# Performance work log

Measured on AMD Instinct MI355X. Metric: run time of the kernel, lower is better.

## Reference

```python
import jax, jax.numpy as jnp
import numpy as np

N_NODES = 100000
N_EDGES = 300000
N_GRAPHS = 2048
F_ATOM = 40
D_IN = 128    # GINInputSize
D_HID = 256   # GINHiddenSize
D_OUT = 512   # FPSize
D_TASK = 1    # OutputSize


def _glorot(key, shape):
    fan_in, fan_out = shape[0], shape[1]
    lim = (6.0 / (fan_in + fan_out)) ** 0.5
    return jax.random.uniform(key, shape, jnp.float32, -lim, lim)


def setup_inputs() -> dict:
    key = jax.random.key(0)
    ks = jax.random.split(key, 16)
    inp = {
        'x': jax.random.normal(ks[0], (N_NODES, F_ATOM), jnp.float32),
        'edge_index': jax.random.randint(ks[1], (2, N_EDGES), 0, N_NODES, jnp.int64),
        'batch': jnp.sort(jax.random.randint(ks[2], (N_NODES,), 0, N_GRAPHS, jnp.int64)),
        # NodeFeatEmbed: MLP([F_ATOM, D_IN]) == single Linear (plain_last)
        'W_embed': _glorot(ks[3], (F_ATOM, D_IN)),
        'b_embed': jnp.zeros((D_IN,), jnp.float32),
        # GINConv eps per layer (train_eps=False -> 0.0 constants)
        'eps': jnp.zeros((3,), jnp.float32),
        # layer 0: MLP([D_IN, D_HID, D_HID])
        'W1_0': _glorot(ks[4], (D_IN, D_HID)),  'b1_0': jnp.zeros((D_HID,), jnp.float32),
        'W2_0': _glorot(ks[5], (D_HID, D_HID)), 'b2_0': jnp.zeros((D_HID,), jnp.float32),
        # layer 1: MLP([D_HID, D_HID, D_HID])
        'W1_1': _glorot(ks[6], (D_HID, D_HID)), 'b1_1': jnp.zeros((D_HID,), jnp.float32),
        'W2_1': _glorot(ks[7], (D_HID, D_HID)), 'b2_1': jnp.zeros((D_HID,), jnp.float32),
        # layer 2 (last, maps to out_channels=FPSize): MLP([D_HID, D_OUT, D_OUT])
        'W1_2': _glorot(ks[8], (D_HID, D_OUT)), 'b1_2': jnp.zeros((D_OUT,), jnp.float32),
        'W2_2': _glorot(ks[9], (D_OUT, D_OUT)), 'b2_2': jnp.zeros((D_OUT,), jnp.float32),
        # task head
        'W_task': _glorot(ks[10], (D_OUT, D_TASK)),
        'b_task': jnp.zeros((D_TASK,), jnp.float32),
    }
    return inp


def _gin_forward(x, edge_index, batch, W_embed, b_embed, eps, layers, W_task, b_task):
    src, dst = edge_index[0], edge_index[1]
    # NodeFeatEmbed
    h = x @ W_embed + b_embed                                    # [N, D_IN]
    n_layers = len(layers)
    for l, (W1, b1, W2, b2) in enumerate(layers):
        # GINConv: MLP((1+eps)*h + sum_{j->i} h_j)
        agg = jax.ops.segment_sum(h[src], dst, num_segments=N_NODES)
        z = (1.0 + eps[l]) * h + agg
        h = jax.nn.relu(z @ W1 + b1) @ W2 + b2
        if l < n_layers - 1:                                     # inter-layer act (not after last)
            h = jax.nn.relu(h)
    # global_add_pool readout
    pooled = jax.ops.segment_sum(h, batch, num_segments=N_GRAPHS)  # [G, D_OUT]
    return pooled @ W_task + b_task                               # [G, D_TASK]


def reference(x, edge_index, batch, W_embed, b_embed, eps,
              W1_0, b1_0, W2_0, b2_0,
              W1_1, b1_1, W2_1, b2_1,
              W1_2, b1_2, W2_2, b2_2,
              W_task, b_task):
    layers = [(W1_0, b1_0, W2_0, b2_0), (W1_1, b1_1, W2_1, b2_1), (W1_2, b1_2, W2_2, b2_2)]
    return _gin_forward(x, edge_index, batch, W_embed, b_embed, eps, layers, W_task, b_task)
```

## Files before the change

kernel.cpp:

```cpp
#include <hip/hip_runtime.h>

#define N_NODES 100000
#define E_EDGES 300000
#define N_GRAPHS 2048

typedef float  floatx4 __attribute__((ext_vector_type(4)));
typedef short  shortx8 __attribute__((ext_vector_type(8)));

__device__ __forceinline__ float bf2f(unsigned short u) {
  return __uint_as_float(((unsigned int)u) << 16);
}
__device__ __forceinline__ unsigned short f2bf(float f) {
  unsigned int u = __float_as_uint(f);
  u += 0x7FFFu + ((u >> 16) & 1u);
  return (unsigned short)(u >> 16);
}

__device__ __forceinline__ void cp16(const void* g, void* l) {
  __builtin_amdgcn_global_load_lds(
      (const __attribute__((address_space(1))) unsigned int*)g,
      (__attribute__((address_space(3))) unsigned int*)l, 16, 0, 0);
}

struct PrepArgs {
  const float* W[4];
  unsigned short* Wt[4];
  int K[4];
  int N[4];
  const float* We;
  const float* be;
  const float* W1_0;
  unsigned short* WfT;
  const float* W2_2;
  const float* b2_2;
  const float* wtask;
  float* w2v;
  float* c2;
  float* nodedot;
  float* out;
  const float* b_task;
};

__global__ __launch_bounds__(256)
void prep_kernel(PrepArgs a) {
  const int blk = blockIdx.x;
  if (blk < 320) {
    int z, b;
    if (blk < 64)       { z = 0; b = blk; }
    else if (blk < 128) { z = 1; b = blk - 64; }
    else if (blk < 192) { z = 2; b = blk - 128; }
    else                { z = 3; b = blk - 192; }
    const int K = a.K[z], N = a.N[z];
    const int nt = N / 32;
    const int kb = (b / nt) * 32, nb = (b % nt) * 32;
    __shared__ unsigned short tile[32][33];
    const float* W = a.W[z];
    unsigned short* Wt = a.Wt[z];
    const int tx = threadIdx.x & 31, ty = threadIdx.x >> 5;
    for (int r = ty; r < 32; r += 8)
      tile[r][tx] = f2bf(W[(size_t)(kb + r) * N + nb + tx]);
    __syncthreads();
    for (int r = ty; r < 32; r += 8)
      Wt[(size_t)(nb + r) * K + kb + tx] = tile[tx][r];
  } else if (blk < 361) {
    const int k = blk - 320;
    const int n = threadIdx.x;
    if (k < 40) {
      float s = 0.f;
      for (int j = 0; j < 128; j++) s = fmaf(a.We[k * 128 + j], a.W1_0[(size_t)j * 256 + n], s);
      a.WfT[n * 64 + k] = f2bf(s);
    } else {
      float s = 0.f;
      for (int j = 0; j < 128; j++) s = fmaf(a.be[j], a.W1_0[(size_t)j * 256 + n], s);
      a.WfT[n * 64 + 40] = f2bf(s);
      for (int kk = 41; kk < 64; kk++) a.WfT[n * 64 + kk] = 0;
    }
  } else if (blk < 490) {
    const int p = blk - 361;
    const int lane = threadIdx.x & 63;
    const int wave = threadIdx.x >> 6;
    if (p < 128) {
      const int k = p * 4 + wave;
      const float* row = a.W2_2 + (size_t)k * 512 + lane * 8;
      float4 a0 = *(const float4*)(row);
      float4 a1 = *(const float4*)(row + 4);
      float4 w0 = *(const float4*)(a.wtask + lane * 8);
      float4 w1 = *(const float4*)(a.wtask + lane * 8 + 4);
      float s = a0.x * w0.x + a0.y * w0.y + a0.z * w0.z + a0.w * w0.w +
                a1.x * w1.x + a1.y * w1.y + a1.z * w1.z + a1.w * w1.w;
#pragma unroll
      for (int off = 32; off > 0; off >>= 1) s += __shfl_down(s, off);
      if (lane == 0) a.w2v[k] = s;
    } else if (wave == 0) {
      float4 a0 = *(const float4*)(a.b2_2 + lane * 8);
      float4 a1 = *(const float4*)(a.b2_2 + lane * 8 + 4);
      float4 w0 = *(const float4*)(a.wtask + lane * 8);
      float4 w1 = *(const float4*)(a.wtask + lane * 8 + 4);
      float s = a0.x * w0.x + a0.y * w0.y + a0.z * w0.z + a0.w * w0.w +
                a1.x * w1.x + a1.y * w1.y + a1.z * w1.z + a1.w * w1.w;
#pragma unroll
      for (int off = 32; off > 0; off >>= 1) s += __shfl_down(s, off);
      if (lane == 0) *a.c2 = s;
    }
  } else if (blk < 881) {
    int i = (blk - 490) * 256 + threadIdx.x;
    if (i < N_NODES) a.nodedot[i] = 0.f;
  } else {
    int g = (blk - 881) * 256 + threadIdx.x;
    if (g < N_GRAPHS) a.out[g] = a.b_task[0];
  }
}

__global__ __launch_bounds__(256)
void zero_kernel(int* __restrict__ p, int n) {
  int i = blockIdx.x * 256 + threadIdx.x;
  if (i < n) p[i] = 0;
}

__global__ __launch_bounds__(256)
void hist_kernel(const int* __restrict__ ei, int* __restrict__ deg) {
  int e = blockIdx.x * 256 + threadIdx.x;
  if (e < E_EDGES) atomicAdd(&deg[ei[E_EDGES + e]], 1);
}

__global__ __launch_bounds__(256)
void scan_blk_kernel(const int* __restrict__ in, int* __restrict__ out,
                     int* __restrict__ blk_sums, int n_in, int n_out) {
  __shared__ int sm[256];
  const int t = threadIdx.x;
  const int base = blockIdx.x * 1024 + t * 4;
  int d0 = (base + 0 < n_in) ? in[base + 0] : 0;
  int d1 = (base + 1 < n_in) ? in[base + 1] : 0;
  int d2 = (base + 2 < n_in) ? in[base + 2] : 0;
  int d3 = (base + 3 < n_in) ? in[base + 3] : 0;
  int s = d0 + d1 + d2 + d3;
  sm[t] = s;
  __syncthreads();
  for (int off = 1; off < 256; off <<= 1) {
    int v = (t >= off) ? sm[t - off] : 0;
    __syncthreads();
    sm[t] += v;
    __syncthreads();
  }
  int excl = sm[t] - s;
  if (base + 0 < n_out) out[base + 0] = excl;
  if (base + 1 < n_out) out[base + 1] = excl + d0;
  if (base + 2 < n_out) out[base + 2] = excl + d0 + d1;
  if (base + 3 < n_out) out[base + 3] = excl + d0 + d1 + d2;
  if (t == 255 && blk_sums) blk_sums[blockIdx.x] = sm[255];
}

__global__ __launch_bounds__(256)
void scan_fix_kernel(int* __restrict__ row_ptr, const int* __restrict__ blk_off,
                     int* __restrict__ cursor) {
  int i = blockIdx.x * 256 + threadIdx.x;
  if (i <= N_NODES) {
    int v = row_ptr[i] + blk_off[i >> 10];
    row_ptr[i] = v;
    if (i < N_NODES) cursor[i] = v;
  }
}

__global__ __launch_bounds__(256)
void fill_kernel(const int* __restrict__ ei, int* __restrict__ cursor,
                 int* __restrict__ csr_src) {
  int e = blockIdx.x * 256 + threadIdx.x;
  if (e < E_EDGES) {
    int d = ei[E_EDGES + e];
    int slot = atomicAdd(&cursor[d], 1);
    csr_src[slot] = ei[e];
  }
}

__global__ __launch_bounds__(256)
void gatherx_kernel(const float* __restrict__ X, unsigned short* __restrict__ G,
                    const int* __restrict__ row_ptr, const int* __restrict__ csr,
                    const float* __restrict__ eps) {
  const int node = blockIdx.x * 4 + (threadIdx.x >> 6);
  const int lane = threadIdx.x & 63;
  const float sc = 1.0f + eps[0];
  const int e0 = row_ptr[node];
  const int e1 = row_ptr[node + 1];
  float acc = 0.f;
  if (lane < 40) {
    acc = sc * X[(size_t)node * 40 + lane];
    int e = e0;
    for (; e + 4 <= e1; e += 4) {
      int s0 = csr[e], s1 = csr[e + 1], s2 = csr[e + 2], s3 = csr[e + 3];
      float a0 = X[(size_t)s0 * 40 + lane];
      float a1 = X[(size_t)s1 * 40 + lane];
      float a2 = X[(size_t)s2 * 40 + lane];
      float a3 = X[(size_t)s3 * 40 + lane];
      acc += (a0 + a1) + (a2 + a3);
    }
    for (; e < e1; e++)
      acc += X[(size_t)csr[e] * 40 + lane];
  } else if (lane == 40) {
    acc = sc + (float)(e1 - e0);
  }
  G[(size_t)node * 64 + lane] = f2bf(acc);
}

__global__ __launch_bounds__(256)
void gather_kernel(const unsigned short* __restrict__ H, unsigned short* __restrict__ Z,
                   const int* __restrict__ row_ptr, const int* __restrict__ csr,
                   const float* __restrict__ eps, int l) {
  const int node = blockIdx.x * 4 + (threadIdx.x >> 6);
  const int lane = threadIdx.x & 63;
  const float sc = 1.0f + eps[l];
  uint2 hv = *(const uint2*)(H + (size_t)node * 256 + lane * 4);
  float acc[4];
  acc[0] = sc * bf2f((unsigned short)(hv.x & 0xFFFF));
  acc[1] = sc * bf2f((unsigned short)(hv.x >> 16));
  acc[2] = sc * bf2f((unsigned short)(hv.y & 0xFFFF));
  acc[3] = sc * bf2f((unsigned short)(hv.y >> 16));
  const int e0 = row_ptr[node];
  const int e1 = row_ptr[node + 1];
  int e = e0;
  for (; e + 2 <= e1; e += 2) {
    int s0 = csr[e], s1 = csr[e + 1];
    uint2 a = *(const uint2*)(H + (size_t)s0 * 256 + lane * 4);
    uint2 b = *(const uint2*)(H + (size_t)s1 * 256 + lane * 4);
    acc[0] += bf2f((unsigned short)(a.x & 0xFFFF)) + bf2f((unsigned short)(b.x & 0xFFFF));
    acc[1] += bf2f((unsigned short)(a.x >> 16))    + bf2f((unsigned short)(b.x >> 16));
    acc[2] += bf2f((unsigned short)(a.y & 0xFFFF)) + bf2f((unsigned short)(b.y & 0xFFFF));
    acc[3] += bf2f((unsigned short)(a.y >> 16))    + bf2f((unsigned short)(b.y >> 16));
  }
  if (e < e1) {
    int s0 = csr[e];
    uint2 a = *(const uint2*)(H + (size_t)s0 * 256 + lane * 4);
    acc[0] += bf2f((unsigned short)(a.x & 0xFFFF));
    acc[1] += bf2f((unsigned short)(a.x >> 16));
    acc[2] += bf2f((unsigned short)(a.y & 0xFFFF));
    acc[3] += bf2f((unsigned short)(a.y >> 16));
  }
  unsigned short z[4] = {f2bf(acc[0]), f2bf(acc[1]), f2bf(acc[2]), f2bf(acc[3])};
  *(uint2*)(Z + (size_t)node * 256 + lane * 4) = *(uint2*)z;
}

template <int K, int NXL, int MODE>
__global__ __launch_bounds__(256, 4)
void gemm_kernel(const unsigned short* __restrict__ A,
                 const unsigned short* __restrict__ Bt,
                 const float* __restrict__ bias, unsigned short* __restrict__ C,
                 const float* __restrict__ w2v, float* __restrict__ nodedot,
                 int M, int N) {
  const int g = blockIdx.x;
  const int mblk = ((g >> (3 + NXL)) << 3) | (g & 7);
  const int nblk = (g >> 3) & ((1 << NXL) - 1);
  const int m0 = mblk * 128;
  const int n0 = nblk * 128;
  if (m0 >= M) return;

  __shared__ unsigned short smem[2 * 128 * 64];
  unsigned short* As = smem;
  unsigned short* Bs = smem + 128 * 64;
  const int tid = threadIdx.x;
  const int lane = tid & 63;
  const int wave = tid >> 6;
  const int wm = (wave & 1) * 64;
  const int wn = (wave >> 1) * 64;
  const int fr = lane & 15;
  const int fq = lane >> 4;

  floatx4 acc[4][4];
#pragma unroll
  for (int i = 0; i < 4; i++)
#pragma unroll
    for (int j = 0; j < 4; j++) acc[i][j] = (floatx4){0.f, 0.f, 0.f, 0.f};

  const unsigned short* gA[4];
  const unsigned short* gB[4];
  unsigned short* lA[4];
  unsigned short* lB[4];
#pragma unroll
  for (int p = 0; p < 4; p++) {
    int c = p * 256 + wave * 64 + lane;
    int row = c >> 3;
    int q = (c & 7) ^ (row & 7);
    int grA = m0 + row;
    if (grA >= M) grA = M - 1;
    gA[p] = A + (size_t)grA * K + q * 8;
    gB[p] = Bt + (size_t)(n0 + row) * K + q * 8;
    lA[p] = &As[(p * 256 + wave * 64) * 8];
    lB[p] = &Bs[(p * 256 + wave * 64) * 8];
  }

  for (int k0 = 0; k0 < K; k0 += 64) {
#pragma unroll
    for (int p = 0; p < 4; p++) cp16(gA[p] + k0, lA[p]);
#pragma unroll
    for (int p = 0; p < 4; p++) cp16(gB[p] + k0, lB[p]);
    __syncthreads();
#pragma unroll
    for (int s0 = 0; s0 < 2; s0++) {
      shortx8 af[4], bf[4];
#pragma unroll
      for (int i = 0; i < 4; i++)
        af[i] = *(const shortx8*)&As[(wm + i * 16 + fr) * 64 +
                                     (((s0 * 4 + fq) ^ (fr & 7)) * 8)];
#pragma unroll
      for (int j = 0; j < 4; j++)
        bf[j] = *(const shortx8*)&Bs[(wn + j * 16 + fr) * 64 +
                                     (((s0 * 4 + fq) ^ (fr & 7)) * 8)];
#pragma unroll
      for (int i = 0; i < 4; i++)
#pragma unroll
        for (int j = 0; j < 4; j++)
          acc[i][j] = __builtin_amdgcn_mfma_f32_16x16x32_bf16(af[i], bf[j], acc[i][j], 0, 0, 0);
    }
    __syncthreads();
  }

  if (MODE == 3) {
    float wv[4], bj[4];
#pragma unroll
    for (int j = 0; j < 4; j++) {
      int col = n0 + wn + j * 16 + fr;
      wv[j] = w2v[col];
      bj[j] = bias[col];
    }
#pragma unroll
    for (int i = 0; i < 4; i++) {
#pragma unroll
      for (int r = 0; r < 4; r++) {
        float p = 0.f;
#pragma unroll
        for (int j = 0; j < 4; j++) p += fmaxf(acc[i][j][r] + bj[j], 0.f) * wv[j];
#pragma unroll
        for (int off = 1; off < 16; off <<= 1) p += __shfl_xor(p, off);
        if (fr == 0) {
          int row = m0 + wm + i * 16 + fq * 4 + r;
          if (row < M) unsafeAtomicAdd(&nodedot[row], p);
        }
      }
    }
  } else {
    unsigned short* Cs = smem;
#pragma unroll
    for (int j = 0; j < 4; j++) {
      int col = wn + j * 16 + fr;
      float bj = bias[n0 + col];
#pragma unroll
      for (int i = 0; i < 4; i++) {
#pragma unroll
        for (int r = 0; r < 4; r++) {
          int row = wm + i * 16 + fq * 4 + r;
          Cs[row * 128 + col] = f2bf(fmaxf(acc[i][j][r] + bj, 0.f));
        }
      }
    }
    __syncthreads();
    const int rcol = (tid & 15) * 8;
#pragma unroll
    for (int p = 0; p < 8; p++) {
      int row = p * 16 + (tid >> 4);
      int grow = m0 + row;
      if (grow < M) {
        uint4 v = *(const uint4*)&Cs[row * 128 + rcol];
        *(uint4*)&C[(size_t)grow * N + n0 + rcol] = v;
      }
    }
  }
}

__global__ __launch_bounds__(256)
void pool_kernel(const float* __restrict__ nodedot, const int* __restrict__ batch,
                 float* __restrict__ out, const float* __restrict__ c2p) {
  int t = blockIdx.x * 256 + threadIdx.x;
  int i0 = t * 64;
  if (i0 >= N_NODES) return;
  int i1 = i0 + 64;
  if (i1 > N_NODES) i1 = N_NODES;
  const float c2 = *c2p;
  int g = batch[i0];
  float s = 0.f;
  for (int i = i0; i < i1; i++) {
    int gi = batch[i];
    if (gi != g) { unsafeAtomicAdd(&out[g], s); g = gi; s = 0.f; }
    s += nodedot[i] + c2;
  }
  unsafeAtomicAdd(&out[g], s);
}

extern "C" void kernel_launch(void* const* d_in, const int* in_sizes, int n_in,
                              void* d_out, int out_size, void* d_ws, size_t ws_size,
                              hipStream_t stream) {
  const float* x       = (const float*)d_in[0];
  const int*   ei      = (const int*)d_in[1];
  const int*   batch   = (const int*)d_in[2];
  const float* W_embed = (const float*)d_in[3];
  const float* b_embed = (const float*)d_in[4];
  const float* eps     = (const float*)d_in[5];
  const float* W1[3] = {(const float*)d_in[6],  (const float*)d_in[10], (const float*)d_in[14]};
  const float* B1[3] = {(const float*)d_in[7],  (const float*)d_in[11], (const float*)d_in[15]};
  const float* W2[3] = {(const float*)d_in[8],  (const float*)d_in[12], (const float*)d_in[16]};
  const float* B2[3] = {(const float*)d_in[9],  (const float*)d_in[13], (const float*)d_in[17]};
  const float* W_task = (const float*)d_in[18];
  const float* b_task = (const float*)d_in[19];
  float* out = (float*)d_out;

  const size_t OFF_RB  = 51200000;
  const size_t OFF_RZ  = 102400000;
  const size_t OFF_AUX = 153600000;
  if (ws_size < OFF_AUX + 4000000) return;
  unsigned short* RH = (unsigned short*)d_ws;
  unsigned short* RB = (unsigned short*)((char*)d_ws + OFF_RB);
  unsigned short* RZ = (unsigned short*)((char*)d_ws + OFF_RZ);
  char* aux = (char*)d_ws + OFF_AUX;
  int* row_ptr  = (int*)(aux);
  int* cursor   = (int*)(aux + 400016);
  int* csr_src  = (int*)(aux + 800016);
  int* blk_sums = (int*)(aux + 2000016);
  int* blk_off  = (int*)(aux + 2000416);
  float* nodedot = (float*)(aux + 2000816);
  unsigned short* WT = (unsigned short*)(aux + 2400832);
  float* w2v = (float*)(aux + 3200832);
  float* c2  = (float*)(aux + 3202880);
  unsigned short* WfT    = WT;
  unsigned short* Wt2_0  = WT + 32768;
  unsigned short* Wt1_1  = WT + 98304;
  unsigned short* Wt2_1  = WT + 163840;
  unsigned short* Wt1_2  = WT + 229376;

  PrepArgs pa;
  pa.W[0] = W2[0]; pa.Wt[0] = Wt2_0; pa.K[0] = 256; pa.N[0] = 256;
  pa.W[1] = W1[1]; pa.Wt[1] = Wt1_1; pa.K[1] = 256; pa.N[1] = 256;
  pa.W[2] = W2[1]; pa.Wt[2] = Wt2_1; pa.K[2] = 256; pa.N[2] = 256;
  pa.W[3] = W1[2]; pa.Wt[3] = Wt1_2; pa.K[3] = 256; pa.N[3] = 512;
  pa.We = W_embed; pa.be = b_embed; pa.W1_0 = W1[0]; pa.WfT = WfT;
  pa.W2_2 = W2[2]; pa.b2_2 = B2[2]; pa.wtask = W_task; pa.w2v = w2v; pa.c2 = c2;
  pa.nodedot = nodedot; pa.out = out; pa.b_task = b_task;
  prep_kernel<<<889, 256, 0, stream>>>(pa);

  zero_kernel<<<(N_NODES + 255) / 256, 256, 0, stream>>>(cursor, N_NODES);
  hist_kernel<<<(E_EDGES + 255) / 256, 256, 0, stream>>>(ei, cursor);
  scan_blk_kernel<<<98, 256, 0, stream>>>(cursor, row_ptr, blk_sums, N_NODES, N_NODES + 1);
  scan_blk_kernel<<<1, 256, 0, stream>>>(blk_sums, blk_off, nullptr, 98, 98);
  scan_fix_kernel<<<(N_NODES + 256) / 256, 256, 0, stream>>>(row_ptr, blk_off, cursor);
  fill_kernel<<<(E_EDGES + 255) / 256, 256, 0, stream>>>(ei, cursor, csr_src);

  const int MB = (N_NODES + 127) / 128;
  const int MB8 = ((MB + 7) / 8) * 8;

  gatherx_kernel<<<N_NODES / 4, 256, 0, stream>>>(x, RZ, row_ptr, csr_src, eps);
  gemm_kernel<64, 1, 0><<<2 * MB8, 256, 0, stream>>>(RZ, WfT, B1[0], RB, nullptr, nullptr, N_NODES, 256);
  gemm_kernel<256, 1, 0><<<2 * MB8, 256, 0, stream>>>(RB, Wt2_0, B2[0], RH, nullptr, nullptr, N_NODES, 256);

  gather_kernel<<<N_NODES / 4, 256, 0, stream>>>(RH, RZ, row_ptr, csr_src, eps, 1);
  gemm_kernel<256, 1, 0><<<2 * MB8, 256, 0, stream>>>(RZ, Wt1_1, B1[1], RB, nullptr, nullptr, N_NODES, 256);
  gemm_kernel<256, 1, 0><<<2 * MB8, 256, 0, stream>>>(RB, Wt2_1, B2[1], RH, nullptr, nullptr, N_NODES, 256);

  gather_kernel<<<N_NODES / 4, 256, 0, stream>>>(RH, RZ, row_ptr, csr_src, eps, 2);
  gemm_kernel<256, 2, 3><<<4 * MB8, 256, 0, stream>>>(RZ, Wt1_2, B1[2], nullptr, w2v, nodedot, N_NODES, 512);

  pool_kernel<<<((N_NODES + 63) / 64 + 255) / 256, 256, 0, stream>>>(nodedot, batch, out, c2);
}
```

Measured before the change: 439.7 us.

## Fuse two-layer MLP GEMMs per 64-row tile keeping hidden activations in LDS

Replaces the pair of separate GEMM launches per GIN layer with a single kernel that computes relu(zW1+b1) for a 64-row tile, stores it in shared memory, then multiplies by W2 without writing the intermediate to global memory. The last layer is likewise rewritten so each block covers all 512 output columns and reduces the node dot product in registers, which means one atomic per row instead of one per column tile. This removes the intermediate HBM round trip and some launches. In exchange, tiles are smaller (64 rows, full N), weights are re-streamed through LDS in 32-wide K chunks with two barriers each, and occupancy drops to 3 blocks per CU.

```diff
diff --git a/kernel.cpp b/kernel.cpp
--- a/kernel.cpp
+++ b/kernel.cpp
@@ -238,30 +238,59 @@
   *(uint2*)(Z + (size_t)node * 256 + lane * 4) = *(uint2*)z;
 }
 
-template <int K, int NXL, int MODE>
-__global__ __launch_bounds__(256, 4)
-void gemm_kernel(const unsigned short* __restrict__ A,
-                 const unsigned short* __restrict__ Bt,
-                 const float* __restrict__ bias, unsigned short* __restrict__ C,
-                 const float* __restrict__ w2v, float* __restrict__ nodedot,
-                 int M, int N) {
-  const int g = blockIdx.x;
-  const int mblk = ((g >> (3 + NXL)) << 3) | (g & 7);
-  const int nblk = (g >> 3) & ((1 << NXL) - 1);
-  const int m0 = mblk * 128;
-  const int n0 = nblk * 128;
-  if (m0 >= M) return;
-
-  __shared__ unsigned short smem[2 * 128 * 64];
-  unsigned short* As = smem;
-  unsigned short* Bs = smem + 128 * 64;
+template <int K1>
+__global__ __launch_bounds__(256, 3)
+void fused_mlp_kernel(const unsigned short* __restrict__ A,
+                      const unsigned short* __restrict__ W1t,
+                      const float* __restrict__ b1,
+                      const unsigned short* __restrict__ W2t,
+                      const float* __restrict__ b2,
+                      unsigned short* __restrict__ H,
+                      int M) {
+  constexpr int ACH = K1 / 8;
+  constexpr int ZP = (64 * ACH) / 256;
+
+  __shared__ uint4 smem4[3072];
+  unsigned short* Bs = (unsigned short*)smem4;
+  unsigned short* Ts = (unsigned short*)(smem4 + 1024);
+
+  const int m0 = blockIdx.x * 64;
   const int tid = threadIdx.x;
   const int lane = tid & 63;
   const int wave = tid >> 6;
-  const int wm = (wave & 1) * 64;
-  const int wn = (wave >> 1) * 64;
   const int fr = lane & 15;
   const int fq = lane >> 4;
+  const int wn = wave * 64;
+
+#pragma unroll
+  for (int p = 0; p < ZP; p++) {
+    int slot = p * 256 + tid;
+    int row = slot / ACH;
+    int cs = slot % ACH;
+    int cg = cs ^ (row & 7);
+    int grow = m0 + row;
+    if (grow >= M) grow = M - 1;
+    cp16(A + (size_t)grow * K1 + cg * 8, Ts + (size_t)(p * 256 + wn) * 8);
+  }
+
+  const int bn_ = tid >> 2;
+  const int bc_ = tid & 3;
+  const unsigned short* srcW1[4];
+  const unsigned short* srcW2[4];
+#pragma unroll
+  for (int p = 0; p < 4; p++) {
+    int n = p * 64 + bn_;
+    int sw = (bc_ ^ ((n >> 1) & 3)) << 3;
+    srcW1[p] = W1t + (size_t)n * K1 + sw;
+    srcW2[p] = W2t + (size_t)n * 256 + sw;
+  }
+
+  int offB[4];
+#pragma unroll
+  for (int j = 0; j < 4; j++) {
+    int n = wn + j * 16 + fr;
+    offB[j] = n * 32 + ((fq ^ ((n >> 1) & 3)) << 3);
+  }
 
   floatx4 acc[4][4];
 #pragma unroll
@@ -269,99 +298,197 @@
 #pragma unroll
     for (int j = 0; j < 4; j++) acc[i][j] = (floatx4){0.f, 0.f, 0.f, 0.f};
 
-  const unsigned short* gA[4];
-  const unsigned short* gB[4];
-  unsigned short* lA[4];
-  unsigned short* lB[4];
+  for (int k0 = 0; k0 < K1; k0 += 32) {
+#pragma unroll
+    for (int p = 0; p < 4; p++)
+      cp16(srcW1[p] + k0, Bs + (size_t)(p * 256 + wn) * 8);
+    __syncthreads();
+    shortx8 af[4], bv[4];
+    const int kc = k0 >> 3;
+#pragma unroll
+    for (int i = 0; i < 4; i++) {
+      int row = i * 16 + fr;
+      af[i] = *(const shortx8*)&Ts[row * K1 + (((kc + fq) ^ (fr & 7)) << 3)];
+    }
+#pragma unroll
+    for (int j = 0; j < 4; j++) bv[j] = *(const shortx8*)&Bs[offB[j]];
+#pragma unroll
+    for (int i = 0; i < 4; i++)
+#pragma unroll
+      for (int j = 0; j < 4; j++)
+        acc[i][j] = __builtin_amdgcn_mfma_f32_16x16x32_bf16(af[i], bv[j], acc[i][j], 0, 0, 0);
+    __syncthreads();
+  }
+
+#pragma unroll
+  for (int j = 0; j < 4; j++) {
+    int col = wn + j * 16 + fr;
+    float bb = b1[col];
+    int cgc = col >> 3, c7 = col & 7;
+#pragma unroll
+    for (int i = 0; i < 4; i++)
+#pragma unroll
+      for (int r = 0; r < 4; r++) {
+        int row = i * 16 + fq * 4 + r;
+        float v = fmaxf(acc[i][j][r] + bb, 0.f);
+        Ts[row * 256 + (((cgc ^ (row & 7)) << 3) | c7)] = f2bf(v);
+        acc[i][j][r] = 0.f;
+      }
+  }
+
+  for (int k0 = 0; k0 < 256; k0 += 32) {
+#pragma unroll
+    for (int p = 0; p < 4; p++)
+      cp16(srcW2[p] + k0, Bs + (size_t)(p * 256 + wn) * 8);
+    __syncthreads();
+    shortx8 af[4], bv[4];
+    const int kc = k0 >> 3;
+#pragma unroll
+    for (int i = 0; i < 4; i++) {
+      int row = i * 16 + fr;
+      af[i] = *(const shortx8*)&Ts[row * 256 + (((kc + fq) ^ (fr & 7)) << 3)];
+    }
+#pragma unroll
+    for (int j = 0; j < 4; j++) bv[j] = *(const shortx8*)&Bs[offB[j]];
+#pragma unroll
+    for (int i = 0; i < 4; i++)
+#pragma unroll
+      for (int j = 0; j < 4; j++)
+        acc[i][j] = __builtin_amdgcn_mfma_f32_16x16x32_bf16(af[i], bv[j], acc[i][j], 0, 0, 0);
+    __syncthreads();
+  }
+
+#pragma unroll
+  for (int j = 0; j < 4; j++) {
+    int col = wn + j * 16 + fr;
+    float bb = b2[col];
+    int cgc = col >> 3, c7 = col & 7;
+#pragma unroll
+    for (int i = 0; i < 4; i++)
+#pragma unroll
+      for (int r = 0; r < 4; r++) {
+        int row = i * 16 + fq * 4 + r;
+        float v = fmaxf(acc[i][j][r] + bb, 0.f);
+        Ts[row * 256 + (((cgc ^ (row & 7)) << 3) | c7)] = f2bf(v);
+      }
+  }
+  __syncthreads();
+  const int r2 = tid >> 5;
+  const int cg2 = tid & 31;
+#pragma unroll
+  for (int p = 0; p < 8; p++) {
+    int row = p * 8 + r2;
+    int grow = m0 + row;
+    if (grow < M) {
+      uint4 v = *(const uint4*)&Ts[row * 256 + ((cg2 ^ (row & 7)) << 3)];
+      *(uint4*)&H[(size_t)grow * 256 + cg2 * 8] = v;
+    }
+  }
+}
+
+__global__ __launch_bounds__(256, 3)
+void fused_dot_kernel(const unsigned short* __restrict__ A,
+                      const unsigned short* __restrict__ W1t,
+                      const float* __restrict__ b1,
+                      const float* __restrict__ w2v,
+                      float* __restrict__ nodedot, int M) {
+  __shared__ uint4 smem4[3072];
+  unsigned short* Bs = (unsigned short*)smem4;
+  unsigned short* Ts = (unsigned short*)(smem4 + 1024);
+
+  const int m0 = blockIdx.x * 64;
+  const int tid = threadIdx.x;
+  const int lane = tid & 63;
+  const int wave = tid >> 6;
+  const int fr = lane & 15;
+  const int fq = lane >> 4;
+  const int wn = wave * 64;
+
+#pragma unroll
+  for (int p = 0; p < 8; p++) {
+    int slot = p * 256 + tid;
+    int row = slot >> 5;
+    int cs = slot & 31;
+    int cg = cs ^ (row & 7);
+    int grow = m0 + row;
+    if (grow >= M) grow = M - 1;
+    cp16(A + (size_t)grow * 256 + cg * 8, Ts + (size_t)(p * 256 + wn) * 8);
+  }
+
+  const int bn_ = tid >> 2;
+  const int bc_ = tid & 3;
+  const unsigned short* srcW[4];
 #pragma unroll
   for (int p = 0; p < 4; p++) {
-    int c = p * 256 + wave * 64 + lane;
-    int row = c >> 3;
-    int q = (c & 7) ^ (row & 7);
-    int grA = m0 + row;
-    if (grA >= M) grA = M - 1;
-    gA[p] = A + (size_t)grA * K + q * 8;
-    gB[p] = Bt + (size_t)(n0 + row) * K + q * 8;
-    lA[p] = &As[(p * 256 + wave * 64) * 8];
-    lB[p] = &Bs[(p * 256 + wave * 64) * 8];
-  }
-
-  for (int k0 = 0; k0 < K; k0 += 64) {
-#pragma unroll
-    for (int p = 0; p < 4; p++) cp16(gA[p] + k0, lA[p]);
-#pragma unroll
-    for (int p = 0; p < 4; p++) cp16(gB[p] + k0, lB[p]);
-    __syncthreads();
-#pragma unroll
-    for (int s0 = 0; s0 < 2; s0++) {
-      shortx8 af[4], bf[4];
+    int n = p * 64 + bn_;
+    srcW[p] = W1t + (size_t)n * 256 + ((bc_ ^ ((n >> 1) & 3)) << 3);
+  }
+  int offB[4];
+#pragma unroll
+  for (int j = 0; j < 4; j++) {
+    int n = wn + j * 16 + fr;
+    offB[j] = n * 32 + ((fq ^ ((n >> 1) & 3)) << 3);
+  }
+
+  float pd[4][4];
+#pragma unroll
+  for (int i = 0; i < 4; i++)
+#pragma unroll
+    for (int r = 0; r < 4; r++) pd[i][r] = 0.f;
+
+  for (int nh = 0; nh < 2; nh++) {
+    floatx4 acc[4][4];
+#pragma unroll
+    for (int i = 0; i < 4; i++)
+#pragma unroll
+      for (int j = 0; j < 4; j++) acc[i][j] = (floatx4){0.f, 0.f, 0.f, 0.f};
+    const size_t nhoff = (size_t)nh * 256 * 256;
+    for (int k0 = 0; k0 < 256; k0 += 32) {
+#pragma unroll
+      for (int p = 0; p < 4; p++)
+        cp16(srcW[p] + nhoff + k0, Bs + (size_t)(p * 256 + wn) * 8);
+      __syncthreads();
+      shortx8 af[4], bv[4];
+      const int kc = k0 >> 3;
+#pragma unroll
+      for (int i = 0; i < 4; i++) {
+        int row = i * 16 + fr;
+        af[i] = *(const shortx8*)&Ts[row * 256 + (((kc + fq) ^ (fr & 7)) << 3)];
+      }
+#pragma unroll
+      for (int j = 0; j < 4; j++) bv[j] = *(const shortx8*)&Bs[offB[j]];
 #pragma unroll
       for (int i = 0; i < 4; i++)
-        af[i] = *(const shortx8*)&As[(wm + i * 16 + fr) * 64 +
-                                     (((s0 * 4 + fq) ^ (fr & 7)) * 8)];
-#pragma unroll
-      for (int j = 0; j < 4; j++)
-        bf[j] = *(const shortx8*)&Bs[(wn + j * 16 + fr) * 64 +
-                                     (((s0 * 4 + fq) ^ (fr & 7)) * 8)];
+#pragma unroll
+        for (int j = 0; j < 4; j++)
+          acc[i][j] = __builtin_amdgcn_mfma_f32_16x16x32_bf16(af[i], bv[j], acc[i][j], 0, 0, 0);
+      __syncthreads();
+    }
+#pragma unroll
+    for (int j = 0; j < 4; j++) {
+      int col = nh * 256 + wn + j * 16 + fr;
+      float bb = b1[col];
+      float wv = w2v[col];
 #pragma unroll
       for (int i = 0; i < 4; i++)
 #pragma unroll
-        for (int j = 0; j < 4; j++)
-          acc[i][j] = __builtin_amdgcn_mfma_f32_16x16x32_bf16(af[i], bf[j], acc[i][j], 0, 0, 0);
-    }
-    __syncthreads();
-  }
-
-  if (MODE == 3) {
-    float wv[4], bj[4];
-#pragma unroll
-    for (int j = 0; j < 4; j++) {
-      int col = n0 + wn + j * 16 + fr;
-      wv[j] = w2v[col];
-      bj[j] = bias[col];
-    }
-#pragma unroll
-    for (int i = 0; i < 4; i++) {
-#pragma unroll
-      for (int r = 0; r < 4; r++) {
-        float p = 0.f;
-#pragma unroll
-        for (int j = 0; j < 4; j++) p += fmaxf(acc[i][j][r] + bj[j], 0.f) * wv[j];
-#pragma unroll
-        for (int off = 1; off < 16; off <<= 1) p += __shfl_xor(p, off);
-        if (fr == 0) {
-          int row = m0 + wm + i * 16 + fq * 4 + r;
-          if (row < M) unsafeAtomicAdd(&nodedot[row], p);
-        }
+        for (int r = 0; r < 4; r++)
+          pd[i][r] += fmaxf(acc[i][j][r] + bb, 0.f) * wv;
+    }
+  }
+
+#pragma unroll
+  for (int i = 0; i < 4; i++)
+#pragma unroll
+    for (int r = 0; r < 4; r++) {
+      float s = pd[i][r];
+#pragma unroll
+      for (int off = 1; off < 16; off <<= 1) s += __shfl_xor(s, off);
+      if (fr == 0) {
+        int row = m0 + i * 16 + fq * 4 + r;
+        if (row < M) unsafeAtomicAdd(&nodedot[row], s);
       }
     }
-  } else {
-    unsigned short* Cs = smem;
-#pragma unroll
-    for (int j = 0; j < 4; j++) {
-      int col = wn + j * 16 + fr;
-      float bj = bias[n0 + col];
-#pragma unroll
-      for (int i = 0; i < 4; i++) {
-#pragma unroll
-        for (int r = 0; r < 4; r++) {
-          int row = wm + i * 16 + fq * 4 + r;
-          Cs[row * 128 + col] = f2bf(fmaxf(acc[i][j][r] + bj, 0.f));
-        }
-      }
-    }
-    __syncthreads();
-    const int rcol = (tid & 15) * 8;
-#pragma unroll
-    for (int p = 0; p < 8; p++) {
-      int row = p * 16 + (tid >> 4);
-      int grow = m0 + row;
-      if (grow < M) {
-        uint4 v = *(const uint4*)&Cs[row * 128 + rcol];
-        *(uint4*)&C[(size_t)grow * N + n0 + rcol] = v;
-      }
-    }
-  }
 }
 
 __global__ __launch_bounds__(256)
@@ -400,12 +527,10 @@
   const float* b_task = (const float*)d_in[19];
   float* out = (float*)d_out;
 
-  const size_t OFF_RB  = 51200000;
   const size_t OFF_RZ  = 102400000;
   const size_t OFF_AUX = 153600000;
   if (ws_size < OFF_AUX + 4000000) return;
   unsigned short* RH = (unsigned short*)d_ws;
-  unsigned short* RB = (unsigned short*)((char*)d_ws + OFF_RB);
   unsigned short* RZ = (unsigned short*)((char*)d_ws + OFF_RZ);
   char* aux = (char*)d_ws + OFF_AUX;
   int* row_ptr  = (int*)(aux);
@@ -440,19 +565,16 @@
   scan_fix_kernel<<<(N_NODES + 256) / 256, 256, 0, stream>>>(row_ptr, blk_off, cursor);
   fill_kernel<<<(E_EDGES + 255) / 256, 256, 0, stream>>>(ei, cursor, csr_src);
 
-  const int MB = (N_NODES + 127) / 128;
-  const int MB8 = ((MB + 7) / 8) * 8;
+  const int FB = (N_NODES + 63) / 64;
 
   gatherx_kernel<<<N_NODES / 4, 256, 0, stream>>>(x, RZ, row_ptr, csr_src, eps);
-  gemm_kernel<64, 1, 0><<<2 * MB8, 256, 0, stream>>>(RZ, WfT, B1[0], RB, nullptr, nullptr, N_NODES, 256);
-  gemm_kernel<256, 1, 0><<<2 * MB8, 256, 0, stream>>>(RB, Wt2_0, B2[0], RH, nullptr, nullptr, N_NODES, 256);
+  fused_mlp_kernel<64><<<FB, 256, 0, stream>>>(RZ, WfT, B1[0], Wt2_0, B2[0], RH, N_NODES);
 
   gather_kernel<<<N_NODES / 4, 256, 0, stream>>>(RH, RZ, row_ptr, csr_src, eps, 1);
-  gemm_kernel<256, 1, 0><<<2 * MB8, 256, 0, stream>>>(RZ, Wt1_1, B1[1], RB, nullptr, nullptr, N_NODES, 256);
-  gemm_kernel<256, 1, 0><<<2 * MB8, 256, 0, stream>>>(RB, Wt2_1, B2[1], RH, nullptr, nullptr, N_NODES, 256);
+  fused_mlp_kernel<256><<<FB, 256, 0, stream>>>(RZ, Wt1_1, B1[1], Wt2_1, B2[1], RH, N_NODES);
 
   gather_kernel<<<N_NODES / 4, 256, 0, stream>>>(RH, RZ, row_ptr, csr_src, eps, 2);
-  gemm_kernel<256, 2, 3><<<4 * MB8, 256, 0, stream>>>(RZ, Wt1_2, B1[2], nullptr, w2v, nodedot, N_NODES, 512);
+  fused_dot_kernel<<<FB, 256, 0, stream>>>(RZ, Wt1_2, B1[2], w2v, nodedot, N_NODES);
 
   pool_kernel<<<((N_NODES + 63) / 64 + 255) / 256, 256, 0, stream>>>(nodedot, batch, out, c2);
 }
```

Result: faster. 422.0 us (-4.0%).
